# Kernel tuning notes

Measured on AMD Instinct MI355X. Metric: run time of the kernel, lower is better.

## Reference

```python
import jax, jax.numpy as jnp
import numpy as np


def _aggregate(xyz, node, features, k):
    # xyz: [B,3,N], node: [B,3,M], features: [B,C,N] -> [B,C,M]
    # squared euclidean distances via expansion (same math as (x-n)^2 sum)
    d = (jnp.sum(xyz ** 2, axis=1)[:, :, None]
         + jnp.sum(node ** 2, axis=1)[:, None, :]
         - 2.0 * jnp.einsum('bdn,bdm->bnm', xyz, node))  # [B,N,M]
    # k smallest over N for each of M nodes (order irrelevant: max-pool after)
    _, nn_idx = jax.lax.top_k(-jnp.transpose(d, (0, 2, 1)), k)  # [B,M,k]
    # gather C-channel features at neighbor indices -> [B,C,M,k]
    g = jnp.take_along_axis(features[:, :, None, :], nn_idx[:, None, :, :], axis=3)
    return jnp.max(g, axis=3)  # [B,C,M]


def setup_inputs() -> dict:
    key = jax.random.key(0)
    k1, k2, k3, k4 = jax.random.split(key, 4)
    B, N, C = 4, 16384, 128
    return {
        'input_coords': jax.random.normal(k1, (B, 3, N), dtype=jnp.float32),
        'input_feats': jax.random.normal(k2, (B, C, N), dtype=jnp.float32),
        'W': jax.random.normal(k3, (C, C), dtype=jnp.float32) * 0.05,
        'b': jax.random.normal(k4, (C,), dtype=jnp.float32) * 0.05,
        'num_sample': 2048,
        'num_agg': 16,
    }


def reference(input_coords, input_feats, W, b, num_sample, num_agg):
    # Dropout in eval mode -> identity. proj = 1x1 Conv1d == per-point linear.
    Z = input_feats  # [B,C,N]
    proj = jax.nn.relu(jnp.einsum('oc,bcn->bon', W, Z) + b[None, :, None])
    vector = jnp.max(proj, axis=-1, keepdims=True)  # [B,C,1]
    weights = jnp.sum(input_feats * vector, axis=1)  # [B,N]
    scores = jax.nn.sigmoid(weights)
    values, idx = jax.lax.top_k(scores, num_sample)  # [B,M] each, sorted desc
    pool_coords_static = jnp.take_along_axis(input_coords, idx[:, None, :], axis=2)  # [B,3,M]
    pool_feats_static = jnp.take_along_axis(input_feats, idx[:, None, :], axis=2)    # [B,C,M]
    v = values[:, None, :]  # [B,1,M]
    pool_feats = pool_feats_static * v
    pool_coords = pool_coords_static * v
    agg_feats = _aggregate(input_coords, pool_coords_static, input_feats, num_agg)  # [B,C,M]
    pool_feats = jnp.concatenate([pool_feats, agg_feats], axis=1)  # [B,2C,M]
    return (pool_coords_static, pool_coords, pool_feats)
```

## Files before the change

### kernel.cpp

```cpp
#include <hip/hip_runtime.h>
#include <hip/hip_bf16.h>
#include <stdint.h>

#define BB 4
#define NN 16384
#define CC 128
#define MM 2048
#define KNN 16
#define QCAP 512
#define EPS 1e-3f

typedef unsigned int u32;
typedef unsigned short u16;
typedef unsigned long long u64;

#define OFF_FEATT   0ull
#define OFF_PTS4    33554432ull
#define OFF_WT      37748736ull
#define OFF_KEYS    37814272ull
#define OFF_VEC     38338560ull
#define OFF_IDX     38340608ull
#define OFF_VAL     38373376ull
#define OFF_TMP1    38406144ull
#define OFF_TMP2    38668288ull

__device__ __forceinline__ float np_dist(float4 p, float4 nd) {
#pragma clang fp contract(off)
    float dot = ((p.x * nd.x) + (p.y * nd.y)) + (p.z * nd.z);
    float d = (p.w + nd.w) - 2.0f * dot;
    return d;
}

__device__ __forceinline__ float sfast(float4 p, float4 nd) {
    float dot = fmaf(p.x, nd.x, fmaf(p.y, nd.y, p.z * nd.z));
    return fmaf(-2.0f, dot, p.w);
}

__device__ __forceinline__ u32 mono_bits(float d) {
    u32 u = __float_as_uint(d);
    u ^= ((u32)(((int)u) >> 31)) | 0x80000000u;
    return u;
}

__device__ __forceinline__ float kth16(float v, int l) {
    float sv = v;
#pragma unroll
    for (int k = 2; k <= 64; k <<= 1) {
#pragma unroll
        for (int j = k >> 1; j > 0; j >>= 1) {
            float pv = __shfl_xor(sv, j);
            bool up = ((l & k) == 0);
            bool tmin = (((l & j) == 0) == up);
            float mn = fminf(sv, pv), mx = fmaxf(sv, pv);
            sv = tmin ? mn : mx;
        }
    }
    return __shfl(sv, 15);
}

__global__ void k_prep(const float* __restrict__ coords, const float* __restrict__ W,
                       float4* __restrict__ pts4, float* __restrict__ WT,
                       u32* __restrict__ vecU) {
    int g = blockIdx.x * 256 + threadIdx.x;
    if (g < BB * NN) {
        int b = g >> 14, n = g & (NN - 1);
        const float* cb = coords + (size_t)b * 3 * NN;
        float x = cb[n], y = cb[NN + n], z = cb[2 * NN + n];
        float w;
        {
#pragma clang fp contract(off)
            w = ((x * x) + (y * y)) + (z * z);
        }
        pts4[g] = make_float4(x, y, z, w);
    } else if (g < BB * NN + CC * CC) {
        int i = g - BB * NN;
        int o = i >> 7, c = i & 127;
        WT[c * CC + o] = W[i];
    } else if (g < BB * NN + CC * CC + BB * CC) {
        vecU[g - BB * NN - CC * CC] = 0u;
    }
}

__global__ void k_transpose(const float* __restrict__ feats, float* __restrict__ feat_t) {
    __shared__ float t[64][65];
    int bx = blockIdx.x;
    int b = bx >> 9; int rem = bx & 511; int nb = rem >> 1; int cb2 = rem & 1;
    int n0 = nb * 64, c0 = cb2 * 64;
    int l = threadIdx.x & 63, r0 = threadIdx.x >> 6;
    const float* fb = feats + (size_t)b * CC * NN;
#pragma unroll
    for (int p = 0; p < 16; ++p) {
        int r = r0 + p * 4;
        t[r][l] = fb[(size_t)(c0 + r) * NN + n0 + l];
    }
    __syncthreads();
    float* ob = feat_t + (size_t)b * NN * CC;
#pragma unroll
    for (int p = 0; p < 16; ++p) {
        int r = r0 + p * 4;
        ob[(size_t)(n0 + r) * CC + c0 + l] = t[l][r];
    }
}

__global__ __launch_bounds__(256) void k_vec(const float* __restrict__ feat_t,
        const float* __restrict__ WT, const float* __restrict__ bias, u32* __restrict__ vecU) {
    int bx = blockIdx.x;
    int b = bx >> 8; int n0 = (bx & 255) * 64;
    int tid = threadIdx.x, l = tid & 63;
    int w = __builtin_amdgcn_readfirstlane(tid >> 6);
    int oh = (w & 1) << 6;
    int ng = w >> 1;
    int o = oh + l;
    const float* zt = feat_t + ((size_t)b * NN + n0 + ng * 32) * CC;
    float bo = bias[o];
    float acc[32];
#pragma unroll
    for (int ni = 0; ni < 32; ++ni) acc[ni] = bo;
    for (int c0 = 0; c0 < CC; c0 += 32) {
        float Wreg[32];
#pragma unroll
        for (int ci = 0; ci < 32; ++ci) Wreg[ci] = WT[(size_t)(c0 + ci) * CC + o];
#pragma unroll
        for (int ni = 0; ni < 32; ++ni) {
            const float* zr = zt + ni * CC + c0;
            float a = acc[ni];
#pragma unroll
            for (int ci = 0; ci < 32; ++ci) a = fmaf(zr[ci], Wreg[ci], a);
            acc[ni] = a;
        }
    }
    float mx = 0.0f;
#pragma unroll
    for (int ni = 0; ni < 32; ++ni) {
        float rv = acc[ni] > 0.0f ? acc[ni] : 0.0f;
        mx = fmaxf(mx, rv);
    }
    atomicMax(vecU + b * CC + o, __float_as_uint(mx));
}

__global__ void k_scores(const float* __restrict__ feats, const float* __restrict__ vecF,
                         u64* __restrict__ keys) {
    int i = blockIdx.x * 256 + threadIdx.x;
    int b = i >> 14, n = i & (NN - 1);
    const float* fb = feats + (size_t)b * CC * NN + n;
    const float* vb = vecF + b * CC;
    float wsum = 0.f;
#pragma unroll 8
    for (int c = 0; c < CC; ++c) wsum = fmaf(fb[(size_t)c * NN], vb[c], wsum);
    float s = 1.0f / (1.0f + expf(-wsum));
    u32 mono = __float_as_uint(s);
    keys[i] = ((u64)mono << 32) | (u64)(0xFFFFFFFFu - (u32)n);
}

__global__ __launch_bounds__(1024) void k_sortchunk(u64* __restrict__ keys) {
    __shared__ u64 sk[2048];
    int b = blockIdx.x >> 3, c = blockIdx.x & 7;
    int tid = threadIdx.x;
    u64* src = keys + (size_t)b * NN + c * 2048;
    sk[tid] = src[tid];
    sk[tid + 1024] = src[tid + 1024];
    for (int size = 2; size <= 2048; size <<= 1) {
        for (int stride = size >> 1; stride > 0; stride >>= 1) {
            __syncthreads();
            int t = tid;
            int i = (t << 1) - (t & (stride - 1));
            int j = i + stride;
            u64 a = sk[i], cc = sk[j];
            bool up = ((i & size) == 0);
            if ((a < cc) == up) { sk[i] = cc; sk[j] = a; }
        }
    }
    __syncthreads();
    src[tid] = sk[tid];
    src[tid + 1024] = sk[tid + 1024];
}

__global__ __launch_bounds__(512) void k_mergetop(const u64* __restrict__ in,
        u64* __restrict__ outp, int lg ) {
    __shared__ u64 mk[4096];
    int b = blockIdx.x >> lg, pr = blockIdx.x & ((1 << lg) - 1);
    int tid = threadIdx.x;
    const u64* s0 = in + ((size_t)((b << lg) + pr) * 2) * 2048;
    const u64* s1 = s0 + 2048;
    for (int t = tid; t < 2048; t += 512) { mk[t] = s0[t]; mk[2048 + t] = s1[2047 - t]; }
    __syncthreads();
    for (int t = tid; t < 2048; t += 512) {
        u64 a = mk[t], c = mk[t + 2048];
        if (a < c) { mk[t] = c; mk[t + 2048] = a; }
    }
    for (int stride = 1024; stride > 0; stride >>= 1) {
        __syncthreads();
        for (int t = tid; t < 1024; t += 512) {
            int i = (t << 1) - (t & (stride - 1));
            int j = i + stride;
            u64 a = mk[i], c = mk[j];
            if (a < c) { mk[i] = c; mk[j] = a; }
        }
    }
    __syncthreads();
    u64* dst = outp + (size_t)((b << lg) + pr) * 2048;
    for (int t = tid; t < 2048; t += 512) dst[t] = mk[t];
}

__global__ __launch_bounds__(512) void k_mergefinal(const u64* __restrict__ in,
        u32* __restrict__ idxA, float* __restrict__ valA) {
    __shared__ u64 mk[4096];
    int b = blockIdx.x, tid = threadIdx.x;
    const u64* s0 = in + (size_t)(b * 2) * 2048;
    const u64* s1 = s0 + 2048;
    for (int t = tid; t < 2048; t += 512) { mk[t] = s0[t]; mk[2048 + t] = s1[2047 - t]; }
    __syncthreads();
    for (int t = tid; t < 2048; t += 512) {
        u64 a = mk[t], c = mk[t + 2048];
        if (a < c) { mk[t] = c; mk[t + 2048] = a; }
    }
    for (int stride = 1024; stride > 0; stride >>= 1) {
        __syncthreads();
        for (int t = tid; t < 1024; t += 512) {
            int i = (t << 1) - (t & (stride - 1));
            int j = i + stride;
            u64 a = mk[i], c = mk[j];
            if (a < c) { mk[i] = c; mk[j] = a; }
        }
    }
    __syncthreads();
    for (int t = tid; t < 2048; t += 512) {
        u64 k = mk[t];
        idxA[b * MM + t] = 0xFFFFFFFFu - (u32)(k & 0xFFFFFFFFull);
        valA[b * MM + t] = __uint_as_float((u32)(k >> 32));
    }
}

__global__ void k_gather(const float4* __restrict__ pts4, const float* __restrict__ feat_t,
        const u32* __restrict__ idxA, const float* __restrict__ valA, float* __restrict__ out) {
    int g = blockIdx.x * 256 + threadIdx.x;
    int b = g >> 11, i = g & (MM - 1);
    u32 n = idxA[g];
    float v = valA[g];
    float4 p = pts4[(b << 14) + (int)n];
    float* o0 = out + (size_t)b * 3 * MM + i;
    o0[0] = p.x; o0[MM] = p.y; o0[2 * MM] = p.z;
    float* o1 = o0 + 24576;
    o1[0] = p.x * v; o1[MM] = p.y * v; o1[2 * MM] = p.z * v;
    const float4* ft = (const float4*)(feat_t + ((size_t)(b << 14) + n) * CC);
    float* o2 = out + 49152 + ((size_t)b * 256) * MM + i;
#pragma unroll 8
    for (int q = 0; q < 32; ++q) {
        float4 f = ft[q];
        o2[(size_t)(4 * q + 0) * MM] = f.x * v;
        o2[(size_t)(4 * q + 1) * MM] = f.y * v;
        o2[(size_t)(4 * q + 2) * MM] = f.z * v;
        o2[(size_t)(4 * q + 3) * MM] = f.w * v;
    }
}

__global__ __launch_bounds__(256, 7) void k_knn(const float4* __restrict__ pts4,
        const float* __restrict__ feat_t, const u32* __restrict__ idxA, float* __restrict__ out) {
    __shared__ float4 ptsS[1024];
    __shared__ u16 qS[4][QCAP];
    __shared__ float4 nodeS[4];
    int bx = blockIdx.x;
    int b = bx >> 9, mblk = bx & 511;
    int tid = threadIdx.x, l = tid & 63;
    const float4* pb = pts4 + (b << 14);
    if (tid < 4) nodeS[tid] = pb[idxA[b * MM + mblk * 4 + tid]];
#pragma unroll
    for (int j = 0; j < 4; ++j) ptsS[tid + 256 * j] = pb[tid + 256 * j];
    __syncthreads();
    int w = __builtin_amdgcn_readfirstlane(tid >> 6);
    float4 nd = nodeS[w];
    float lm = 3.0e38f;
#pragma unroll 4
    for (int j = 0; j < 16; ++j) lm = fminf(lm, sfast(ptsS[l + 64 * j], nd));
    __syncthreads();
#pragma unroll
    for (int j = 0; j < 4; ++j) ptsS[tid + 256 * j] = pb[1024 + tid + 256 * j];
    __syncthreads();
#pragma unroll 4
    for (int j = 0; j < 16; ++j) lm = fminf(lm, sfast(ptsS[l + 64 * j], nd));
    float T = kth16(lm, l) + 2.0f * EPS;
    int qc = 0;
    for (int ch = 0; ch < 16; ++ch) {
        __syncthreads();
#pragma unroll
        for (int j = 0; j < 4; ++j) ptsS[tid + 256 * j] = pb[ch * 1024 + tid + 256 * j];
        __syncthreads();
        for (int j = 0; j < 16; ++j) {
            float4 p = ptsS[l + 64 * j];
            float dt = fmaf(p.x, nd.x, fmaf(p.y, nd.y, p.z * nd.z));
            float s = fmaf(-2.0f, dt, p.w);
            bool pred = (s <= T);
            u64 bal = __ballot(pred);
            if (bal) {
                if (pred) {
                    int off = __builtin_amdgcn_mbcnt_hi((u32)(bal >> 32),
                              __builtin_amdgcn_mbcnt_lo((u32)bal, 0));
                    int slot = qc + off;
                    if (slot < QCAP) qS[w][slot] = (u16)(ch * 1024 + l + 64 * j);
                }
                qc += (int)__popcll(bal);
            }
        }
    }
    int cnt = qc < QCAP ? qc : QCAP;
    u64 regk[QCAP / 64];
#pragma unroll
    for (int s = 0; s < QCAP / 64; ++s) {
        u64 kk = ~0ull;
        if ((s << 6) < cnt) {
            int pos = (s << 6) + l;
            if (pos < cnt) {
                u32 n = qS[w][pos];
                float d = np_dist(pb[n], nd);
                kk = ((u64)mono_bits(d) << 32) | (u64)n;
            }
        }
        regk[s] = kk;
    }
    float mx0 = -3.0e38f, mx1 = -3.0e38f;
    for (int it = 0; it < KNN; ++it) {
        u64 mykey = ~0ull;
#pragma unroll
        for (int s = 0; s < QCAP / 64; ++s)
            if ((s << 6) < cnt) mykey = regk[s] < mykey ? regk[s] : mykey;
        u64 r = mykey;
#pragma unroll
        for (int j = 32; j > 0; j >>= 1) {
            u64 o = __shfl_xor(r, j);
            r = o < r ? o : r;
        }
#pragma unroll
        for (int s = 0; s < QCAP / 64; ++s)
            if ((s << 6) < cnt) { if (regk[s] == r) regk[s] = ~0ull; }
        if (r != ~0ull) {
            u32 nj = (u32)(r & 0xFFFFFFFFull);
            const float2 f = *(const float2*)(feat_t + ((size_t)(b << 14) + nj) * CC + (l << 1));
            mx0 = fmaxf(mx0, f.x);
            mx1 = fmaxf(mx1, f.y);
        }
    }
    int m = mblk * 4 + w;
    size_t ob = 49152 + ((size_t)(b * 256 + 128 + 2 * l)) * MM + m;
    out[ob] = mx0;
    out[ob + MM] = mx1;
}

extern "C" void kernel_launch(void* const* d_in, const int* in_sizes, int n_in,
                              void* d_out, int out_size, void* d_ws, size_t ws_size,
                              hipStream_t stream) {
    const float* coords = (const float*)d_in[0];
    const float* feats  = (const float*)d_in[1];
    const float* W      = (const float*)d_in[2];
    const float* bias   = (const float*)d_in[3];
    char* ws = (char*)d_ws;
    float*  feat_t = (float*)(ws + OFF_FEATT);
    float4* pts4   = (float4*)(ws + OFF_PTS4);
    float*  WT     = (float*)(ws + OFF_WT);
    u64*    keys   = (u64*)(ws + OFF_KEYS);
    u32*    vecU   = (u32*)(ws + OFF_VEC);
    u32*    idxA   = (u32*)(ws + OFF_IDX);
    float*  valA   = (float*)(ws + OFF_VAL);
    u64*    tmp1   = (u64*)(ws + OFF_TMP1);
    u64*    tmp2   = (u64*)(ws + OFF_TMP2);
    float*  out    = (float*)d_out;

    int prepN = BB * NN + CC * CC + BB * CC;
    k_prep     <<<(prepN + 255) / 256, 256, 0, stream>>>(coords, W, pts4, WT, vecU);
    k_transpose<<<BB * (NN / 64) * (CC / 64), 256, 0, stream>>>(feats, feat_t);
    k_vec      <<<BB * (NN / 64), 256, 0, stream>>>(feat_t, WT, bias, vecU);
    k_scores   <<<BB * NN / 256, 256, 0, stream>>>(feats, (const float*)vecU, keys);
    k_sortchunk<<<BB * 8, 1024, 0, stream>>>(keys);
    k_mergetop <<<BB * 4, 512, 0, stream>>>(keys, tmp1, 2);
    k_mergetop <<<BB * 2, 512, 0, stream>>>(tmp1, tmp2, 1);
    k_mergefinal<<<BB, 512, 0, stream>>>(tmp2, idxA, valA);
    k_gather   <<<BB * MM / 256, 256, 0, stream>>>(pts4, feat_t, idxA, valA, out);
    k_knn      <<<BB * (MM / 4), 256, 0, stream>>>(pts4, feat_t, idxA, out);
}
```

Measured before the change: 288.7 us.

## Rework projection-max kernel to read untransposed features with lane-per-point mapping

The projection/max kernel now reads features directly in [B,C,N] layout, one point per lane, and each wave computes 32 output channels. Weights are wave-uniform float4 loads that are software-prefetched one channel ahead. Before the atomic, the max is reduced across the wave with shuffles, so only one atomic per channel per wave is issued. The kernel no longer depends on the transposed buffer, so it is launched before the transpose. This gives coalesced loads and fewer atomics, at the cost of a serial one-channel-at-a-time loop with a small amount of FMA work per load.

```diff
diff --git a/kernel.cpp b/kernel.cpp
--- a/kernel.cpp
+++ b/kernel.cpp
@@ -102,40 +102,56 @@
     }
 }
 
-__global__ __launch_bounds__(256) void k_vec(const float* __restrict__ feat_t,
+__global__ __launch_bounds__(256) void k_vec(const float* __restrict__ feats,
         const float* __restrict__ WT, const float* __restrict__ bias, u32* __restrict__ vecU) {
     int bx = blockIdx.x;
     int b = bx >> 8; int n0 = (bx & 255) * 64;
     int tid = threadIdx.x, l = tid & 63;
-    int w = __builtin_amdgcn_readfirstlane(tid >> 6);
-    int oh = (w & 1) << 6;
-    int ng = w >> 1;
-    int o = oh + l;
-    const float* zt = feat_t + ((size_t)b * NN + n0 + ng * 32) * CC;
-    float bo = bias[o];
+    int q = __builtin_amdgcn_readfirstlane(tid >> 6);
+    int o0 = q * 32;
+    const float* fb = feats + (size_t)b * CC * NN + n0 + l;
+    const float4* wt = (const float4*)(WT + o0);
     float acc[32];
 #pragma unroll
-    for (int ni = 0; ni < 32; ++ni) acc[ni] = bo;
-    for (int c0 = 0; c0 < CC; c0 += 32) {
-        float Wreg[32];
-#pragma unroll
-        for (int ci = 0; ci < 32; ++ci) Wreg[ci] = WT[(size_t)(c0 + ci) * CC + o];
-#pragma unroll
-        for (int ni = 0; ni < 32; ++ni) {
-            const float* zr = zt + ni * CC + c0;
-            float a = acc[ni];
-#pragma unroll
-            for (int ci = 0; ci < 32; ++ci) a = fmaf(zr[ci], Wreg[ci], a);
-            acc[ni] = a;
-        }
-    }
-    float mx = 0.0f;
-#pragma unroll
-    for (int ni = 0; ni < 32; ++ni) {
-        float rv = acc[ni] > 0.0f ? acc[ni] : 0.0f;
-        mx = fmaxf(mx, rv);
-    }
-    atomicMax(vecU + b * CC + o, __float_as_uint(mx));
+    for (int oi = 0; oi < 32; ++oi) acc[oi] = bias[o0 + oi];
+    float4 wb0 = wt[0], wb1 = wt[1], wb2 = wt[2], wb3 = wt[3];
+    float4 wb4 = wt[4], wb5 = wt[5], wb6 = wt[6], wb7 = wt[7];
+    float zb = fb[0];
+#pragma unroll 1
+    for (int c = 0; c < CC; ++c) {
+        float4 w0 = wb0, w1 = wb1, w2 = wb2, w3 = wb3;
+        float4 w4 = wb4, w5 = wb5, w6 = wb6, w7 = wb7;
+        float zc = zb;
+        if (c + 1 < CC) {
+            const float4* wn = wt + (c + 1) * 32;
+            wb0 = wn[0]; wb1 = wn[1]; wb2 = wn[2]; wb3 = wn[3];
+            wb4 = wn[4]; wb5 = wn[5]; wb6 = wn[6]; wb7 = wn[7];
+            zb = fb[(size_t)(c + 1) * NN];
+        }
+        acc[0]  = fmaf(w0.x, zc, acc[0]);  acc[1]  = fmaf(w0.y, zc, acc[1]);
+        acc[2]  = fmaf(w0.z, zc, acc[2]);  acc[3]  = fmaf(w0.w, zc, acc[3]);
+        acc[4]  = fmaf(w1.x, zc, acc[4]);  acc[5]  = fmaf(w1.y, zc, acc[5]);
+        acc[6]  = fmaf(w1.z, zc, acc[6]);  acc[7]  = fmaf(w1.w, zc, acc[7]);
+        acc[8]  = fmaf(w2.x, zc, acc[8]);  acc[9]  = fmaf(w2.y, zc, acc[9]);
+        acc[10] = fmaf(w2.z, zc, acc[10]); acc[11] = fmaf(w2.w, zc, acc[11]);
+        acc[12] = fmaf(w3.x, zc, acc[12]); acc[13] = fmaf(w3.y, zc, acc[13]);
+        acc[14] = fmaf(w3.z, zc, acc[14]); acc[15] = fmaf(w3.w, zc, acc[15]);
+        acc[16] = fmaf(w4.x, zc, acc[16]); acc[17] = fmaf(w4.y, zc, acc[17]);
+        acc[18] = fmaf(w4.z, zc, acc[18]); acc[19] = fmaf(w4.w, zc, acc[19]);
+        acc[20] = fmaf(w5.x, zc, acc[20]); acc[21] = fmaf(w5.y, zc, acc[21]);
+        acc[22] = fmaf(w5.z, zc, acc[22]); acc[23] = fmaf(w5.w, zc, acc[23]);
+        acc[24] = fmaf(w6.x, zc, acc[24]); acc[25] = fmaf(w6.y, zc, acc[25]);
+        acc[26] = fmaf(w6.z, zc, acc[26]); acc[27] = fmaf(w6.w, zc, acc[27]);
+        acc[28] = fmaf(w7.x, zc, acc[28]); acc[29] = fmaf(w7.y, zc, acc[29]);
+        acc[30] = fmaf(w7.z, zc, acc[30]); acc[31] = fmaf(w7.w, zc, acc[31]);
+    }
+#pragma unroll
+    for (int oi = 0; oi < 32; ++oi) {
+        float rv = acc[oi] > 0.0f ? acc[oi] : 0.0f;
+#pragma unroll
+        for (int s = 32; s; s >>= 1) rv = fmaxf(rv, __shfl_xor(rv, s));
+        if (l == 0) atomicMax(vecU + b * CC + o0 + oi, __float_as_uint(rv));
+    }
 }
 
 __global__ void k_scores(const float* __restrict__ feats, const float* __restrict__ vecF,
@@ -366,8 +382,8 @@
 
     int prepN = BB * NN + CC * CC + BB * CC;
     k_prep     <<<(prepN + 255) / 256, 256, 0, stream>>>(coords, W, pts4, WT, vecU);
+    k_vec      <<<BB * (NN / 64), 256, 0, stream>>>(feats, WT, bias, vecU);
     k_transpose<<<BB * (NN / 64) * (CC / 64), 256, 0, stream>>>(feats, feat_t);
-    k_vec      <<<BB * (NN / 64), 256, 0, stream>>>(feat_t, WT, bias, vecU);
     k_scores   <<<BB * NN / 256, 256, 0, stream>>>(feats, (const float*)vecU, keys);
     k_sortchunk<<<BB * 8, 1024, 0, stream>>>(keys);
     k_mergetop <<<BB * 4, 512, 0, stream>>>(keys, tmp1, 2);
```

After: 348.1 us. +20.6%, slower.
